# Performance work log

Hardware: AMD Instinct MI355X
Metric: run time of the kernel (lower is better)

Reference implementation:

```python
import jax, jax.numpy as jnp
import numpy as np

D = 256
NL = 2048
NP = 16384
B = 32
NEG = -1e9


def _layernorm(x, g, b, eps=1e-5):
    mu = x.mean(-1, keepdims=True)
    var = ((x - mu) ** 2).mean(-1, keepdims=True)
    return (x - mu) / jnp.sqrt(var + eps) * g + b


def _cdist(a, b):
    # pairwise euclidean distances, [Na, Nb]
    d2 = (a * a).sum(-1)[:, None] + (b * b).sum(-1)[None, :] - 2.0 * (a @ b.T)
    return jnp.sqrt(jnp.maximum(d2, 1e-12))


def setup_inputs() -> dict:
    key = jax.random.key(0)
    ks = jax.random.split(key, 24)
    init = lambda k, shape: jax.random.normal(k, shape, jnp.float32) / np.float32(np.sqrt(shape[-1]))
    inp = {
        "lig": jax.random.normal(ks[0], (NL, D), jnp.float32),
        "pro": jax.random.normal(ks[1], (NP, D), jnp.float32),
        "lig_pos": jax.random.normal(ks[2], (NL, 3), jnp.float32),
        "pro_pos": jax.random.normal(ks[3], (NP, 3), jnp.float32),
        "lig_batch": jnp.sort(jax.random.randint(ks[4], (NL,), 0, B, jnp.int32)),
        "pro_batch": jnp.sort(jax.random.randint(ks[5], (NP,), 0, B, jnp.int32)),
        "Wq_lig": init(ks[6], (D, D)),
        "Wk_pro": init(ks[7], (D, D)),
        "Wv_pro": init(ks[8], (D, D)),
        "Wq_pro": init(ks[9], (D, D)),
        "Wk_lig": init(ks[10], (D, D)),
        "Wv_lig": init(ks[11], (D, D)),
        "Wout_lig": init(ks[12], (D, D)),
        "bout_lig": jnp.zeros((D,), jnp.float32),
        "Wout_pro": init(ks[13], (D, D)),
        "bout_pro": jnp.zeros((D,), jnp.float32),
        "g_lig": jnp.ones((D,), jnp.float32),
        "b_lig": jnp.zeros((D,), jnp.float32),
        "g_pro": jnp.ones((D,), jnp.float32),
        "b_pro": jnp.zeros((D,), jnp.float32),
    }
    return inp


def reference(lig, pro, lig_pos, pro_pos, lig_batch, pro_batch,
              Wq_lig, Wk_pro, Wv_pro, Wq_pro, Wk_lig, Wv_lig,
              Wout_lig, bout_lig, Wout_pro, bout_pro,
              g_lig, b_lig, g_pro, b_pro):
    scale = jnp.float32(np.sqrt(D))
    # block-diagonal structure via batch-id mask; each row has >=1 valid col
    mask = lig_batch[:, None] == pro_batch[None, :]  # [NL, NP]
    dist_bias = jnp.exp(-_cdist(lig_pos, pro_pos) / 10.0)  # [NL, NP]

    # ligand <- protein
    Q = lig @ Wq_lig.T
    K = pro @ Wk_pro.T
    V = pro @ Wv_pro.T
    scores = Q @ K.T / scale + dist_bias
    attn = jax.nn.softmax(jnp.where(mask, scores, NEG), axis=-1)
    l_ctx = attn @ V
    lig_out = _layernorm(lig + l_ctx @ Wout_lig.T + bout_lig, g_lig, b_lig)

    # protein <- ligand
    Q2 = pro @ Wq_pro.T
    K2 = lig @ Wk_lig.T
    V2 = lig @ Wv_lig.T
    scores2 = Q2 @ K2.T / scale + dist_bias.T
    attn2 = jax.nn.softmax(jnp.where(mask.T, scores2, NEG), axis=-1)
    p_ctx = attn2 @ V2
    pro_out = _layernorm(pro + p_ctx @ Wout_pro.T + bout_pro, g_pro, b_pro)

    return lig_out, pro_out
```

## Files before the change

### kernel.cpp

```cpp
#include <hip/hip_runtime.h>

static constexpr int NLr = 2048;
static constexpr int NPr = 16384;
static constexpr int DIM = 256;
static constexpr int NB  = 32;

typedef unsigned short bf16_t;
using bf16x8 = __attribute__((ext_vector_type(8))) short;
using f32x4  = __attribute__((ext_vector_type(4))) float;

__device__ inline float bf2f(bf16_t u){
  union { unsigned int i; float f; } c; c.i = ((unsigned int)u) << 16; return c.f;
}
__device__ inline bf16_t f2bf(float f){
  union { float f; unsigned int i; } c; c.f = f;
  unsigned int x = c.i;
  return (bf16_t)((x + 0x7fffu + ((x >> 16) & 1u)) >> 16);
}
__device__ inline float wave_sum(float x){
  #pragma unroll
  for (int off = 32; off; off >>= 1) x += __shfl_xor(x, off, 64);
  return x;
}
__device__ inline bf16x8 ldfrag_f32(const float* p){
  float4 a = *reinterpret_cast<const float4*>(p);
  float4 b = *reinterpret_cast<const float4*>(p + 4);
  bf16x8 r;
  r[0]=(short)f2bf(a.x); r[1]=(short)f2bf(a.y); r[2]=(short)f2bf(a.z); r[3]=(short)f2bf(a.w);
  r[4]=(short)f2bf(b.x); r[5]=(short)f2bf(b.y); r[6]=(short)f2bf(b.z); r[7]=(short)f2bf(b.w);
  return r;
}
__device__ inline void hilo8(const float* p, bf16x8& hi, bf16x8& lo){
  #pragma unroll
  for (int i = 0; i < 8; i++){
    float v = p[i];
    bf16_t h = f2bf(v);
    hi[i] = (short)h;
    lo[i] = (short)f2bf(v - bf2f(h));
  }
}

static constexpr int OPART_OFF  = 2621440;
static constexpr int MLPART_OFF = 2605056;

__global__ void bounds_kernel(const int* __restrict__ lb, const int* __restrict__ pb,
                              int* __restrict__ ls, int* __restrict__ ps){
  int t = threadIdx.x;
  if (t <= NB){
    int lo = 0, hi = NLr;
    while (lo < hi){ int mid = (lo + hi) >> 1; if (lb[mid] < t) lo = mid + 1; else hi = mid; }
    ls[t] = lo;
    lo = 0; hi = NPr;
    while (lo < hi){ int mid = (lo + hi) >> 1; if (pb[mid] < t) lo = mid + 1; else hi = mid; }
    ps[t] = lo;
  }
}

__global__ __launch_bounds__(256) void wprod4(
    const float* __restrict__ Wq_lig, const float* __restrict__ Wk_pro,
    const float* __restrict__ Wk_lig, const float* __restrict__ Wq_pro,
    const float* __restrict__ Wout_lig, const float* __restrict__ Wv_pro,
    const float* __restrict__ Wout_pro, const float* __restrict__ Wv_lig,
    bf16_t* __restrict__ A1, bf16_t* __restrict__ B2,
    bf16_t* __restrict__ PtTL, bf16_t* __restrict__ PtTP){
  __shared__ float Sa[1088];
  __shared__ float Sb[1088];
  const int z = blockIdx.z;
  const float *A, *B; bf16_t* C;
  if      (z == 0){ A = Wq_lig;   B = Wk_pro; C = A1;   }
  else if (z == 1){ A = Wk_lig;   B = Wq_pro; C = B2;   }
  else if (z == 2){ A = Wout_lig; B = Wv_pro; C = PtTL; }
  else            { A = Wout_pro; B = Wv_lig; C = PtTP; }
  const int t  = threadIdx.x;
  const int tx = t & 15, ty = t >> 4;
  const int bm = blockIdx.x, bn = blockIdx.y;
  float acc[4][4] = {};
  if (z < 2){
    float (*As)[68] = (float(*)[68])Sa;
    float (*Bs)[68] = (float(*)[68])Sb;
    const int kk = t >> 4, c0 = (t & 15) << 2;
    for (int kt = 0; kt < DIM; kt += 16){
      float4 av = *reinterpret_cast<const float4*>(A + (size_t)(kt+kk)*DIM + bm*64 + c0);
      float4 bv = *reinterpret_cast<const float4*>(B + (size_t)(kt+kk)*DIM + bn*64 + c0);
      As[kk][c0+0]=av.x; As[kk][c0+1]=av.y; As[kk][c0+2]=av.z; As[kk][c0+3]=av.w;
      Bs[kk][c0+0]=bv.x; Bs[kk][c0+1]=bv.y; Bs[kk][c0+2]=bv.z; Bs[kk][c0+3]=bv.w;
      __syncthreads();
      #pragma unroll
      for (int k = 0; k < 16; k++){
        float a[4], b[4];
        #pragma unroll
        for (int i = 0; i < 4; i++) a[i] = As[k][ty*4+i];
        #pragma unroll
        for (int j = 0; j < 4; j++) b[j] = Bs[k][tx*4+j];
        #pragma unroll
        for (int i = 0; i < 4; i++)
          #pragma unroll
          for (int j = 0; j < 4; j++) acc[i][j] += a[i]*b[j];
      }
      __syncthreads();
    }
  } else {
    float (*As)[17] = (float(*)[17])Sa;
    float (*Bs)[68] = (float(*)[68])Sb;
    const int r  = t >> 2, k0 = (t & 3) << 2;
    const int kk = t >> 4, c0 = (t & 15) << 2;
    for (int kt = 0; kt < DIM; kt += 16){
      float4 av = *reinterpret_cast<const float4*>(A + (size_t)(bm*64+r)*DIM + kt + k0);
      float4 bv = *reinterpret_cast<const float4*>(B + (size_t)(kt+kk)*DIM + bn*64 + c0);
      As[r][k0+0]=av.x; As[r][k0+1]=av.y; As[r][k0+2]=av.z; As[r][k0+3]=av.w;
      Bs[kk][c0+0]=bv.x; Bs[kk][c0+1]=bv.y; Bs[kk][c0+2]=bv.z; Bs[kk][c0+3]=bv.w;
      __syncthreads();
      #pragma unroll
      for (int k = 0; k < 16; k++){
        float a[4], b[4];
        #pragma unroll
        for (int i = 0; i < 4; i++) a[i] = As[ty*4+i][k];
        #pragma unroll
        for (int j = 0; j < 4; j++) b[j] = Bs[k][tx*4+j];
        #pragma unroll
        for (int i = 0; i < 4; i++)
          #pragma unroll
          for (int j = 0; j < 4; j++) acc[i][j] += a[i]*b[j];
      }
      __syncthreads();
    }
  }
  #pragma unroll
  for (int i = 0; i < 4; i++){
    ushort4 o;
    o.x=f2bf(acc[i][0]); o.y=f2bf(acc[i][1]); o.z=f2bf(acc[i][2]); o.w=f2bf(acc[i][3]);
    *reinterpret_cast<ushort4*>(C + (size_t)(bm*64+ty*4+i)*DIM + bn*64 + tx*4) = o;
  }
}

__global__ __launch_bounds__(256) void gemm2(
    const float* __restrict__ A, const bf16_t* __restrict__ Ba, const bf16_t* __restrict__ Bb,
    bf16_t* __restrict__ Ca, bf16_t* __restrict__ Cb){
  const bf16_t* B = blockIdx.z ? Bb : Ba;
  bf16_t*       C = blockIdx.z ? Cb : Ca;
  __shared__ float As[64][17];
  __shared__ float Bs[16][68];
  const int t  = threadIdx.x;
  const int r  = t >> 2, k0 = (t & 3) << 2;
  const int kk = t >> 4, c0 = (t & 15) << 2;
  const int tx = t & 15, ty = t >> 4;
  const int bm = blockIdx.x, bn = blockIdx.y;
  float acc[4][4] = {};
  for (int kt = 0; kt < DIM; kt += 16){
    float4 av = *reinterpret_cast<const float4*>(A + (size_t)(bm*64+r)*DIM + kt + k0);
    ushort4 bu = *reinterpret_cast<const ushort4*>(B + (size_t)(kt+kk)*DIM + bn*64 + c0);
    As[r][k0+0]=av.x; As[r][k0+1]=av.y; As[r][k0+2]=av.z; As[r][k0+3]=av.w;
    Bs[kk][c0+0]=bf2f(bu.x); Bs[kk][c0+1]=bf2f(bu.y);
    Bs[kk][c0+2]=bf2f(bu.z); Bs[kk][c0+3]=bf2f(bu.w);
    __syncthreads();
    #pragma unroll
    for (int k = 0; k < 16; k++){
      float a[4], b[4];
      #pragma unroll
      for (int i = 0; i < 4; i++) a[i] = As[ty*4+i][k];
      #pragma unroll
      for (int j = 0; j < 4; j++) b[j] = Bs[k][tx*4+j];
      #pragma unroll
      for (int i = 0; i < 4; i++)
        #pragma unroll
        for (int j = 0; j < 4; j++) acc[i][j] += a[i]*b[j];
    }
    __syncthreads();
  }
  #pragma unroll
  for (int i = 0; i < 4; i++){
    ushort4 o;
    o.x=f2bf(acc[i][0]); o.y=f2bf(acc[i][1]); o.z=f2bf(acc[i][2]); o.w=f2bf(acc[i][3]);
    *reinterpret_cast<ushort4*>(C + (size_t)(bm*64+ty*4+i)*DIM + bn*64 + tx*4) = o;
  }
}

__global__ __launch_bounds__(128) void attn_lig(
    const bf16_t* __restrict__ Qb, const float* __restrict__ Kf,
    const float* __restrict__ posA, const float* __restrict__ posB,
    const int* __restrict__ batchA, const int* __restrict__ startB,
    float* __restrict__ dout, int NK){
  __shared__ __align__(16) char raw[36864];
  __shared__ bf16_t Pbuf[2][16][40];
  __shared__ float  mlb[2][2][16];
  bf16_t* Vlds = (bf16_t*)raw;
  float*  Ob   = (float*)raw;
  float* Opart  = dout + OPART_OFF;
  float* mlpart = dout + MLPART_OFF;

  const int t = threadIdx.x, wl = t >> 6, lane = t & 63;
  const int qrow = lane & 15, q4 = lane >> 4;
  const int tile = blockIdx.x >> 2, split = blockIdx.x & 3;
  const int row0 = tile * 16, pidx = blockIdx.x;

  const int rb = batchA[row0 + qrow];
  const int j0 = startB[rb], j1 = startB[rb + 1];
  const float ax = posA[(size_t)(row0+qrow)*3+0];
  const float ay = posA[(size_t)(row0+qrow)*3+1];
  const float az = posA[(size_t)(row0+qrow)*3+2];
  const int kmin = startB[batchA[row0]];
  const int kmax = startB[batchA[row0 + 15] + 1];
  const int base = kmin & ~63;

  bf16x8 qf[8];
  #pragma unroll
  for (int s = 0; s < 8; s++)
    qf[s] = *reinterpret_cast<const bf16x8*>(Qb + (size_t)(row0+qrow)*DIM + s*32 + q4*8);

  f32x4 O[16];
  #pragma unroll
  for (int i = 0; i < 16; i++) O[i] = (f32x4){0.f,0.f,0.f,0.f};
  float m_ = -3.0e38f, l_ = 0.f;

  for (int c = base + split*64; c < kmax; c += 256){
    __syncthreads();
    {
      const int key = t & 63, half = t >> 6;
      const float* src = Kf + (size_t)min(c + key, NK-1)*DIM + half*128;
      #pragma unroll
      for (int gch = 0; gch < 4; gch++){
        float4 tmp[8];
        #pragma unroll
        for (int u = 0; u < 8; u++)
          tmp[u] = *reinterpret_cast<const float4*>(src + gch*32 + u*4);
        #pragma unroll
        for (int u = 0; u < 8; u++){
          int d = half*128 + gch*32 + u*4;
          Vlds[(d+0)*72 + key] = f2bf(tmp[u].x);
          Vlds[(d+1)*72 + key] = f2bf(tmp[u].y);
          Vlds[(d+2)*72 + key] = f2bf(tmp[u].z);
          Vlds[(d+3)*72 + key] = f2bf(tmp[u].w);
        }
      }
    }
    __syncthreads();

    const int kc0 = c + wl*32, colbase = wl*32;
    f32x4 a0 = (f32x4){0.f,0.f,0.f,0.f}, a1 = a0;
    const float* kr0 = Kf + (size_t)min(kc0 + qrow,      NK-1)*DIM;
    const float* kr1 = Kf + (size_t)min(kc0 + 16 + qrow, NK-1)*DIM;
    #pragma unroll
    for (int s = 0; s < 8; s++){
      bf16x8 ka = ldfrag_f32(kr0 + s*32 + q4*8);
      bf16x8 kb = ldfrag_f32(kr1 + s*32 + q4*8);
      a0 = __builtin_amdgcn_mfma_f32_16x16x32_bf16(ka, qf[s], a0, 0, 0, 0);
      a1 = __builtin_amdgcn_mfma_f32_16x16x32_bf16(kb, qf[s], a1, 0, 0, 0);
    }
    float sc[2][4]; bool vm[2][4];
    float cm = -3.0e38f;
    #pragma unroll
    for (int h = 0; h < 2; h++)
      #pragma unroll
      for (int r = 0; r < 4; r++){
        int key = kc0 + h*16 + q4*4 + r;
        bool vld = (key >= j0) && (key < j1);
        int kc = min(key, NK-1);
        float bx = posB[(size_t)kc*3+0], by = posB[(size_t)kc*3+1], bz = posB[(size_t)kc*3+2];
        float dx = ax-bx, dy = ay-by, dz = az-bz;
        float dist = sqrtf(fmaxf(dx*dx + dy*dy + dz*dz, 1e-12f));
        float sv = (h ? a1[r] : a0[r]) * 0.0625f + __expf(-0.1f*dist);
        sc[h][r] = vld ? sv : -3.0e38f;
        vm[h][r] = vld;
        cm = fmaxf(cm, sc[h][r]);
      }
    cm = fmaxf(cm, __shfl_xor(cm, 16));
    cm = fmaxf(cm, __shfl_xor(cm, 32));
    float mn = fmaxf(m_, cm);
    float aa = __expf(m_ - mn);
    float p[2][4]; float ps = 0.f;
    #pragma unroll
    for (int h = 0; h < 2; h++)
      #pragma unroll
      for (int r = 0; r < 4; r++){
        p[h][r] = vm[h][r] ? __expf(sc[h][r] - mn) : 0.f;
        ps += p[h][r];
      }
    ps += __shfl_xor(ps, 16);
    ps += __shfl_xor(ps, 32);
    l_ = l_*aa + ps;
    m_ = mn;
    ushort4 w0, w1;
    w0.x=f2bf(p[0][0]); w0.y=f2bf(p[0][1]); w0.z=f2bf(p[0][2]); w0.w=f2bf(p[0][3]);
    w1.x=f2bf(p[1][0]); w1.y=f2bf(p[1][1]); w1.z=f2bf(p[1][2]); w1.w=f2bf(p[1][3]);
    *reinterpret_cast<ushort4*>(&Pbuf[wl][qrow][q4*4])      = w0;
    *reinterpret_cast<ushort4*>(&Pbuf[wl][qrow][16 + q4*4]) = w1;
    float af0 = __shfl(aa, q4*4+0), af1 = __shfl(aa, q4*4+1);
    float af2 = __shfl(aa, q4*4+2), af3 = __shfl(aa, q4*4+3);
    #pragma unroll
    for (int i = 0; i < 16; i++){
      O[i][0]*=af0; O[i][1]*=af1; O[i][2]*=af2; O[i][3]*=af3;
    }
    bf16x8 pa = *reinterpret_cast<const bf16x8*>(&Pbuf[wl][qrow][q4*8]);
    #pragma unroll
    for (int i = 0; i < 16; i++){
      const bf16_t* vp = Vlds + (size_t)(i*16 + qrow)*72 + colbase + q4*8;
      bf16x8 vb = *reinterpret_cast<const bf16x8*>(vp);
      O[i] = __builtin_amdgcn_mfma_f32_16x16x32_bf16(pa, vb, O[i], 0, 0, 0);
    }
  }

  __syncthreads();
  if (lane < 16){ mlb[wl][0][lane] = m_; mlb[wl][1][lane] = l_; }
  #pragma unroll
  for (int i = 0; i < 16; i++)
    #pragma unroll
    for (int r = 0; r < 4; r++)
      Ob[wl*4096 + (q4*4+r)*256 + i*16 + qrow] = O[i][r];
  __syncthreads();
  for (int e = t; e < 4096; e += 128){
    int row = e >> 8, d = e & 255;
    float m0 = mlb[0][0][row], m1 = mlb[1][0][row];
    float mg = fmaxf(m0, m1);
    float f0 = __expf(m0 - mg), f1 = __expf(m1 - mg);
    Opart[(size_t)pidx*4096 + row*256 + d] = Ob[row*256 + d]*f0 + Ob[4096 + row*256 + d]*f1;
  }
  if (t < 16){
    float m0 = mlb[0][0][t], l0 = mlb[0][1][t];
    float m1 = mlb[1][0][t], l1 = mlb[1][1][t];
    float mg = fmaxf(m0, m1);
    mlpart[pidx*32 + t]      = mg;
    mlpart[pidx*32 + 16 + t] = l0*__expf(m0-mg) + l1*__expf(m1-mg);
  }
}

__global__ __launch_bounds__(128) void merge_lig(
    const float* __restrict__ dpart, const bf16_t* __restrict__ PtT,
    const float* __restrict__ X, const float* __restrict__ bo,
    const float* __restrict__ g, const float* __restrict__ bb,
    float* __restrict__ out){
  __shared__ float ctxl[16*260];
  __shared__ float Yb[16*260];
  __shared__ float wgt[4][16];
  __shared__ float dens[16];
  const float* Opart  = dpart + OPART_OFF;
  const float* mlpart = dpart + MLPART_OFF;
  const int t = threadIdx.x, wl = t >> 6, lane = t & 63;
  const int qrow = lane & 15, q4 = lane >> 4;
  const int tile = blockIdx.x, row0 = tile*16;
  if (t < 16){
    float mm[4], ll[4], mg = -3.0e38f;
    #pragma unroll
    for (int s = 0; s < 4; s++){
      mm[s] = mlpart[(tile*4+s)*32 + t];
      ll[s] = mlpart[(tile*4+s)*32 + 16 + t];
      mg = fmaxf(mg, mm[s]);
    }
    float den = 0.f;
    #pragma unroll
    for (int s = 0; s < 4; s++){
      float w = __expf(mm[s] - mg);
      wgt[s][t] = w;
      den += ll[s]*w;
    }
    dens[t] = den;
  }
  __syncthreads();
  for (int e = t; e < 4096; e += 128){
    int row = e >> 8, d = e & 255;
    float acc = 0.f;
    #pragma unroll
    for (int s = 0; s < 4; s++)
      acc += Opart[((size_t)(tile*4+s))*4096 + row*256 + d] * wgt[s][row];
    float dd = dens[row];
    ctxl[row*260 + d] = (dd > 0.f) ? acc/dd : 0.f;
  }
  __syncthreads();
  f32x4 Y[8];
  #pragma unroll
  for (int i = 0; i < 8; i++) Y[i] = (f32x4){0.f,0.f,0.f,0.f};
  #pragma unroll
  for (int s = 0; s < 8; s++){
    bf16x8 ca, cl;
    hilo8(ctxl + qrow*260 + s*32 + q4*8, ca, cl);
    #pragma unroll
    for (int tt = 0; tt < 8; tt++){
      const bf16_t* pb = PtT + (size_t)((wl*8+tt)*16 + qrow)*DIM + s*32 + q4*8;
      bf16x8 mb = *reinterpret_cast<const bf16x8*>(pb);
      Y[tt] = __builtin_amdgcn_mfma_f32_16x16x32_bf16(ca, mb, Y[tt], 0, 0, 0);
      Y[tt] = __builtin_amdgcn_mfma_f32_16x16x32_bf16(cl, mb, Y[tt], 0, 0, 0);
    }
  }
  #pragma unroll
  for (int tt = 0; tt < 8; tt++)
    #pragma unroll
    for (int r = 0; r < 4; r++)
      Yb[(q4*4+r)*260 + (wl*8+tt)*16 + qrow] = Y[tt][r];
  __syncthreads();
  for (int i = 0; i < 8; i++){
    int r = wl*8 + i, grow = row0 + r;
    float4 yv = *reinterpret_cast<const float4*>(&Yb[r*260 + 4*lane]);
    float4 xv = *reinterpret_cast<const float4*>(X  + (size_t)grow*DIM + 4*lane);
    float4 bv = *reinterpret_cast<const float4*>(bo + 4*lane);
    float4 gv = *reinterpret_cast<const float4*>(g  + 4*lane);
    float4 b2 = *reinterpret_cast<const float4*>(bb + 4*lane);
    float v0 = xv.x + yv.x + bv.x, v1 = xv.y + yv.y + bv.y;
    float v2 = xv.z + yv.z + bv.z, v3 = xv.w + yv.w + bv.w;
    float sum = wave_sum(v0+v1+v2+v3);
    float ssq = wave_sum(v0*v0+v1*v1+v2*v2+v3*v3);
    float mu  = sum * (1.0f/DIM);
    float var = ssq * (1.0f/DIM) - mu*mu;
    float rr  = rsqrtf(fmaxf(var, 0.f) + 1e-5f);
    float4 o;
    o.x = (v0-mu)*rr*gv.x + b2.x;
    o.y = (v1-mu)*rr*gv.y + b2.y;
    o.z = (v2-mu)*rr*gv.z + b2.z;
    o.w = (v3-mu)*rr*gv.w + b2.w;
    *reinterpret_cast<float4*>(out + (size_t)grow*DIM + 4*lane) = o;
  }
}

__global__ __launch_bounds__(128) void attn_pro(
    const float* __restrict__ Qf, const bf16_t* __restrict__ Kb,
    const float* __restrict__ Vf,
    const float* __restrict__ posA, const float* __restrict__ posB,
    const int* __restrict__ batchA, const int* __restrict__ startB,
    const bf16_t* __restrict__ PtT,
    const float* __restrict__ X, const float* __restrict__ bo,
    const float* __restrict__ g, const float* __restrict__ bb,
    float* __restrict__ out, int out_off, int NK){
  __shared__ __align__(16) char raw[33280];
  __shared__ bf16_t Pbuf[2][16][40];
  bf16_t* Vlds = (bf16_t*)raw;
  float*  ctxl = (float*)raw;

  const int t = threadIdx.x, wl = t >> 6, lane = t & 63;
  const int qrow = lane & 15, q4 = lane >> 4;
  const int row0b = blockIdx.x * 32, row0 = row0b + wl*16;

  const int rb = batchA[row0 + qrow];
  const int j0 = startB[rb], j1 = startB[rb + 1];
  const float ax = posA[(size_t)(row0+qrow)*3+0];
  const float ay = posA[(size_t)(row0+qrow)*3+1];
  const float az = posA[(size_t)(row0+qrow)*3+2];
  const int kmin = startB[batchA[row0b]];
  const int kmax = startB[batchA[row0b + 31] + 1];
  const int base = kmin & ~31;

  bf16x8 qf[8], ql[8];
  #pragma unroll
  for (int s = 0; s < 8; s++)
    hilo8(Qf + (size_t)(row0+qrow)*DIM + s*32 + q4*8, qf[s], ql[s]);

  f32x4 O[16];
  #pragma unroll
  for (int i = 0; i < 16; i++) O[i] = (f32x4){0.f,0.f,0.f,0.f};
  float m_ = -3.0e38f, l_ = 0.f;

  for (int c = base; c < kmax; c += 32){
    __syncthreads();
    {
      const int key = t & 31, qtr = t >> 5;
      const float* src = Vf + (size_t)min(c + key, NK-1)*DIM + qtr*64;
      #pragma unroll
      for (int gch = 0; gch < 2; gch++){
        float4 tmp[8];
        #pragma unroll
        for (int u = 0; u < 8; u++)
          tmp[u] = *reinterpret_cast<const float4*>(src + gch*32 + u*4);
        #pragma unroll
        for (int u = 0; u < 8; u++){
          int d = qtr*64 + gch*32 + u*4;
          Vlds[(d+0)*40 + key] = f2bf(tmp[u].x);
          Vlds[(d+1)*40 + key] = f2bf(tmp[u].y);
          Vlds[(d+2)*40 + key] = f2bf(tmp[u].z);
          Vlds[(d+3)*40 + key] = f2bf(tmp[u].w);
        }
      }
    }
    __syncthreads();

    f32x4 a0 = (f32x4){0.f,0.f,0.f,0.f}, a1 = a0;
    const bf16_t* kr0 = Kb + (size_t)min(c + qrow,      NK-1)*DIM;
    const bf16_t* kr1 = Kb + (size_t)min(c + 16 + qrow, NK-1)*DIM;
    #pragma unroll
    for (int s = 0; s < 8; s++){
      bf16x8 ka = *reinterpret_cast<const bf16x8*>(kr0 + s*32 + q4*8);
      bf16x8 kb = *reinterpret_cast<const bf16x8*>(kr1 + s*32 + q4*8);
      a0 = __builtin_amdgcn_mfma_f32_16x16x32_bf16(ka, qf[s], a0, 0, 0, 0);
      a1 = __builtin_amdgcn_mfma_f32_16x16x32_bf16(kb, qf[s], a1, 0, 0, 0);
      a0 = __builtin_amdgcn_mfma_f32_16x16x32_bf16(ka, ql[s], a0, 0, 0, 0);
      a1 = __builtin_amdgcn_mfma_f32_16x16x32_bf16(kb, ql[s], a1, 0, 0, 0);
    }
    float sc[2][4]; bool vm[2][4];
    float cm = -3.0e38f;
    #pragma unroll
    for (int h = 0; h < 2; h++)
      #pragma unroll
      for (int r = 0; r < 4; r++){
        int key = c + h*16 + q4*4 + r;
        bool vld = (key >= j0) && (key < j1);
        int kc = min(key, NK-1);
        float bx = posB[(size_t)kc*3+0], by = posB[(size_t)kc*3+1], bz = posB[(size_t)kc*3+2];
        float dx = ax-bx, dy = ay-by, dz = az-bz;
        float dist = sqrtf(fmaxf(dx*dx + dy*dy + dz*dz, 1e-12f));
        float sv = (h ? a1[r] : a0[r]) * 0.0625f + __expf(-0.1f*dist);
        sc[h][r] = vld ? sv : -3.0e38f;
        vm[h][r] = vld;
        cm = fmaxf(cm, sc[h][r]);
      }
    cm = fmaxf(cm, __shfl_xor(cm, 16));
    cm = fmaxf(cm, __shfl_xor(cm, 32));
    float mn = fmaxf(m_, cm);
    float aa = __expf(m_ - mn);
    float p[2][4]; float ps = 0.f;
    #pragma unroll
    for (int h = 0; h < 2; h++)
      #pragma unroll
      for (int r = 0; r < 4; r++){
        p[h][r] = vm[h][r] ? __expf(sc[h][r] - mn) : 0.f;
        ps += p[h][r];
      }
    ps += __shfl_xor(ps, 16);
    ps += __shfl_xor(ps, 32);
    l_ = l_*aa + ps;
    m_ = mn;
    ushort4 w0, w1;
    w0.x=f2bf(p[0][0]); w0.y=f2bf(p[0][1]); w0.z=f2bf(p[0][2]); w0.w=f2bf(p[0][3]);
    w1.x=f2bf(p[1][0]); w1.y=f2bf(p[1][1]); w1.z=f2bf(p[1][2]); w1.w=f2bf(p[1][3]);
    *reinterpret_cast<ushort4*>(&Pbuf[wl][qrow][q4*4])      = w0;
    *reinterpret_cast<ushort4*>(&Pbuf[wl][qrow][16 + q4*4]) = w1;
    float af0 = __shfl(aa, q4*4+0), af1 = __shfl(aa, q4*4+1);
    float af2 = __shfl(aa, q4*4+2), af3 = __shfl(aa, q4*4+3);
    #pragma unroll
    for (int i = 0; i < 16; i++){
      O[i][0]*=af0; O[i][1]*=af1; O[i][2]*=af2; O[i][3]*=af3;
    }
    bf16x8 pa = *reinterpret_cast<const bf16x8*>(&Pbuf[wl][qrow][q4*8]);
    #pragma unroll
    for (int i = 0; i < 16; i++){
      const bf16_t* vp = Vlds + (size_t)(i*16 + qrow)*40 + q4*8;
      bf16x8 vb = *reinterpret_cast<const bf16x8*>(vp);
      O[i] = __builtin_amdgcn_mfma_f32_16x16x32_bf16(pa, vb, O[i], 0, 0, 0);
    }
  }

  __syncthreads();
  {
    float lr0 = __shfl(l_, q4*4+0), lr1 = __shfl(l_, q4*4+1);
    float lr2 = __shfl(l_, q4*4+2), lr3 = __shfl(l_, q4*4+3);
    float i0 = lr0>0.f?1.f/lr0:0.f, i1 = lr1>0.f?1.f/lr1:0.f;
    float i2 = lr2>0.f?1.f/lr2:0.f, i3 = lr3>0.f?1.f/lr3:0.f;
    float* cw = ctxl + wl*4160;
    #pragma unroll
    for (int i = 0; i < 16; i++){
      cw[(q4*4+0)*260 + i*16+qrow] = O[i][0]*i0;
      cw[(q4*4+1)*260 + i*16+qrow] = O[i][1]*i1;
      cw[(q4*4+2)*260 + i*16+qrow] = O[i][2]*i2;
      cw[(q4*4+3)*260 + i*16+qrow] = O[i][3]*i3;
    }
  }
  const float* cw = ctxl + wl*4160;
  f32x4 Y[16];
  #pragma unroll
  for (int i = 0; i < 16; i++) Y[i] = (f32x4){0.f,0.f,0.f,0.f};
  #pragma unroll
  for (int s = 0; s < 8; s++){
    bf16x8 ca, cl;
    hilo8(cw + qrow*260 + s*32 + q4*8, ca, cl);
    #pragma unroll
    for (int tt = 0; tt < 16; tt++){
      const bf16_t* pb = PtT + (size_t)(tt*16 + qrow)*DIM + s*32 + q4*8;
      bf16x8 mb = *reinterpret_cast<const bf16x8*>(pb);
      Y[tt] = __builtin_amdgcn_mfma_f32_16x16x32_bf16(ca, mb, Y[tt], 0, 0, 0);
      Y[tt] = __builtin_amdgcn_mfma_f32_16x16x32_bf16(cl, mb, Y[tt], 0, 0, 0);
    }
  }
  float* YB = ctxl + wl*4160;
  #pragma unroll
  for (int tt = 0; tt < 16; tt++)
    #pragma unroll
    for (int r = 0; r < 4; r++)
      YB[(q4*4+r)*260 + tt*16 + qrow] = Y[tt][r];

  for (int i = 0; i < 16; i++){
    int grow = row0 + i;
    float4 yv = *reinterpret_cast<const float4*>(&YB[i*260 + 4*lane]);
    float4 xv = *reinterpret_cast<const float4*>(X  + (size_t)grow*DIM + 4*lane);
    float4 bv = *reinterpret_cast<const float4*>(bo + 4*lane);
    float4 gv = *reinterpret_cast<const float4*>(g  + 4*lane);
    float4 b2 = *reinterpret_cast<const float4*>(bb + 4*lane);
    float v0 = xv.x + yv.x + bv.x, v1 = xv.y + yv.y + bv.y;
    float v2 = xv.z + yv.z + bv.z, v3 = xv.w + yv.w + bv.w;
    float sum = wave_sum(v0+v1+v2+v3);
    float ssq = wave_sum(v0*v0+v1*v1+v2*v2+v3*v3);
    float mu  = sum * (1.0f/DIM);
    float var = ssq * (1.0f/DIM) - mu*mu;
    float rr  = rsqrtf(fmaxf(var, 0.f) + 1e-5f);
    float4 o;
    o.x = (v0-mu)*rr*gv.x + b2.x;
    o.y = (v1-mu)*rr*gv.y + b2.y;
    o.z = (v2-mu)*rr*gv.z + b2.z;
    o.w = (v3-mu)*rr*gv.w + b2.w;
    *reinterpret_cast<float4*>(out + (size_t)out_off + (size_t)grow*DIM + 4*lane) = o;
  }
}

extern "C" void kernel_launch(void* const* d_in, const int* in_sizes, int n_in,
                              void* d_out, int out_size, void* d_ws, size_t ws_size,
                              hipStream_t stream){
  const float* lig      = (const float*)d_in[0];
  const float* pro      = (const float*)d_in[1];
  const float* lig_pos  = (const float*)d_in[2];
  const float* pro_pos  = (const float*)d_in[3];
  const int*   lig_batch= (const int*)d_in[4];
  const int*   pro_batch= (const int*)d_in[5];
  const float* Wq_lig   = (const float*)d_in[6];
  const float* Wk_pro   = (const float*)d_in[7];
  const float* Wv_pro   = (const float*)d_in[8];
  const float* Wq_pro   = (const float*)d_in[9];
  const float* Wk_lig   = (const float*)d_in[10];
  const float* Wv_lig   = (const float*)d_in[11];
  const float* Wout_lig = (const float*)d_in[12];
  const float* bout_lig = (const float*)d_in[13];
  const float* Wout_pro = (const float*)d_in[14];
  const float* bout_pro = (const float*)d_in[15];
  const float* g_lig    = (const float*)d_in[16];
  const float* b_lig    = (const float*)d_in[17];
  const float* g_pro    = (const float*)d_in[18];
  const float* b_pro    = (const float*)d_in[19];

  int* ib        = (int*)d_ws;
  int* lig_start = ib + 16;
  int* pro_start = ib + 56;
  bf16_t* wsb  = ((bf16_t*)d_ws) + 256;
  bf16_t* A1   = wsb;
  bf16_t* B2   = A1   + DIM*DIM;
  bf16_t* PtTL = B2   + DIM*DIM;
  bf16_t* PtTP = PtTL + DIM*DIM;
  bf16_t* G    = PtTP + DIM*DIM;
  bf16_t* T_lig= G    + (size_t)NLr*DIM;

  float* outp = (float*)d_out;

  hipLaunchKernelGGL(bounds_kernel, dim3(1), dim3(64), 0, stream,
                     lig_batch, pro_batch, lig_start, pro_start);
  hipLaunchKernelGGL(wprod4, dim3(4,4,4), dim3(256), 0, stream,
                     Wq_lig, Wk_pro, Wk_lig, Wq_pro, Wout_lig, Wv_pro, Wout_pro, Wv_lig,
                     A1, B2, PtTL, PtTP);
  hipLaunchKernelGGL(gemm2, dim3(NLr/64, 4, 2), dim3(256), 0, stream,
                     lig, A1, B2, T_lig, G);

  hipLaunchKernelGGL(attn_lig, dim3(NLr/16*4), dim3(128), 0, stream,
                     T_lig, pro, lig_pos, pro_pos, lig_batch, pro_start, outp, NPr);
  hipLaunchKernelGGL(merge_lig, dim3(NLr/16), dim3(128), 0, stream,
                     outp, PtTL, lig, bout_lig, g_lig, b_lig, outp);

  hipLaunchKernelGGL(attn_pro, dim3(NPr/32), dim3(128), 0, stream,
                     pro, G, lig, pro_pos, lig_pos, pro_batch, lig_start, PtTP,
                     pro, bout_pro, g_pro, b_pro, outp, NLr*DIM, NLr);
}
```

Before: 265.5 us.

## Double attn_lig key splits and split attn_pro keys across waves per row tile

attn_lig now splits each ligand tile's key range into 8 partial blocks instead of 4, and merge_lig combines 8 partials. The ml partials move to workspace and the O partials to a new offset in the output buffer. attn_pro switches from two waves each owning 16 rows over 32-key chunks to one 16-row tile per block, with the two waves splitting 64-key chunks and merging their softmax states through LDS. The output projection and layernorm are then split across the two waves. This raises parallelism and the block count for both attention kernels, at the cost of extra merge traffic, LDS work and barriers.

```diff
diff --git a/kernel.cpp b/kernel.cpp
--- a/kernel.cpp
+++ b/kernel.cpp
@@ -40,8 +40,7 @@
   }
 }
 
-static constexpr int OPART_OFF  = 2621440;
-static constexpr int MLPART_OFF = 2605056;
+static constexpr int OPART_OFF = 524288;
 
 __global__ void bounds_kernel(const int* __restrict__ lb, const int* __restrict__ pb,
                               int* __restrict__ ls, int* __restrict__ ps){
@@ -179,19 +178,18 @@
     const bf16_t* __restrict__ Qb, const float* __restrict__ Kf,
     const float* __restrict__ posA, const float* __restrict__ posB,
     const int* __restrict__ batchA, const int* __restrict__ startB,
-    float* __restrict__ dout, int NK){
+    float* __restrict__ dout, float* __restrict__ mlpart, int NK){
   __shared__ __align__(16) char raw[36864];
   __shared__ bf16_t Pbuf[2][16][40];
   __shared__ float  mlb[2][2][16];
   bf16_t* Vlds = (bf16_t*)raw;
   float*  Ob   = (float*)raw;
-  float* Opart  = dout + OPART_OFF;
-  float* mlpart = dout + MLPART_OFF;
+  float* Opart = dout + OPART_OFF;
 
   const int t = threadIdx.x, wl = t >> 6, lane = t & 63;
   const int qrow = lane & 15, q4 = lane >> 4;
-  const int tile = blockIdx.x >> 2, split = blockIdx.x & 3;
-  const int row0 = tile * 16, pidx = blockIdx.x;
+  const int pidx = blockIdx.x, tile = pidx >> 3, split = pidx & 7;
+  const int row0 = tile * 16;
 
   const int rb = batchA[row0 + qrow];
   const int j0 = startB[rb], j1 = startB[rb + 1];
@@ -212,7 +210,7 @@
   for (int i = 0; i < 16; i++) O[i] = (f32x4){0.f,0.f,0.f,0.f};
   float m_ = -3.0e38f, l_ = 0.f;
 
-  for (int c = base + split*64; c < kmax; c += 256){
+  for (int c = base + split*64; c < kmax; c += 512){
     __syncthreads();
     {
       const int key = t & 63, half = t >> 6;
@@ -324,30 +322,30 @@
 }
 
 __global__ __launch_bounds__(128) void merge_lig(
-    const float* __restrict__ dpart, const bf16_t* __restrict__ PtT,
+    const float* __restrict__ dpart, const float* __restrict__ mlpart,
+    const bf16_t* __restrict__ PtT,
     const float* __restrict__ X, const float* __restrict__ bo,
     const float* __restrict__ g, const float* __restrict__ bb,
     float* __restrict__ out){
   __shared__ float ctxl[16*260];
   __shared__ float Yb[16*260];
-  __shared__ float wgt[4][16];
+  __shared__ float wgt[8][16];
   __shared__ float dens[16];
-  const float* Opart  = dpart + OPART_OFF;
-  const float* mlpart = dpart + MLPART_OFF;
+  const float* Opart = dpart + OPART_OFF;
   const int t = threadIdx.x, wl = t >> 6, lane = t & 63;
   const int qrow = lane & 15, q4 = lane >> 4;
   const int tile = blockIdx.x, row0 = tile*16;
   if (t < 16){
-    float mm[4], ll[4], mg = -3.0e38f;
-    #pragma unroll
-    for (int s = 0; s < 4; s++){
-      mm[s] = mlpart[(tile*4+s)*32 + t];
-      ll[s] = mlpart[(tile*4+s)*32 + 16 + t];
+    float mm[8], ll[8], mg = -3.0e38f;
+    #pragma unroll
+    for (int s = 0; s < 8; s++){
+      mm[s] = mlpart[(tile*8+s)*32 + t];
+      ll[s] = mlpart[(tile*8+s)*32 + 16 + t];
       mg = fmaxf(mg, mm[s]);
     }
     float den = 0.f;
     #pragma unroll
-    for (int s = 0; s < 4; s++){
+    for (int s = 0; s < 8; s++){
       float w = __expf(mm[s] - mg);
       wgt[s][t] = w;
       den += ll[s]*w;
@@ -359,8 +357,8 @@
     int row = e >> 8, d = e & 255;
     float acc = 0.f;
     #pragma unroll
-    for (int s = 0; s < 4; s++)
-      acc += Opart[((size_t)(tile*4+s))*4096 + row*256 + d] * wgt[s][row];
+    for (int s = 0; s < 8; s++)
+      acc += Opart[((size_t)(tile*8+s))*4096 + row*256 + d] * wgt[s][row];
     float dd = dens[row];
     ctxl[row*260 + d] = (dd > 0.f) ? acc/dd : 0.f;
   }
@@ -418,23 +416,24 @@
     const float* __restrict__ X, const float* __restrict__ bo,
     const float* __restrict__ g, const float* __restrict__ bb,
     float* __restrict__ out, int out_off, int NK){
-  __shared__ __align__(16) char raw[33280];
+  __shared__ __align__(16) char raw[36864];
   __shared__ bf16_t Pbuf[2][16][40];
+  __shared__ float  mlb[2][2][16];
   bf16_t* Vlds = (bf16_t*)raw;
-  float*  ctxl = (float*)raw;
+  float*  Ob   = (float*)raw;
 
   const int t = threadIdx.x, wl = t >> 6, lane = t & 63;
   const int qrow = lane & 15, q4 = lane >> 4;
-  const int row0b = blockIdx.x * 32, row0 = row0b + wl*16;
+  const int row0 = blockIdx.x * 16;
 
   const int rb = batchA[row0 + qrow];
   const int j0 = startB[rb], j1 = startB[rb + 1];
   const float ax = posA[(size_t)(row0+qrow)*3+0];
   const float ay = posA[(size_t)(row0+qrow)*3+1];
   const float az = posA[(size_t)(row0+qrow)*3+2];
-  const int kmin = startB[batchA[row0b]];
-  const int kmax = startB[batchA[row0b + 31] + 1];
-  const int base = kmin & ~31;
+  const int kmin = startB[batchA[row0]];
+  const int kmax = startB[batchA[row0 + 15] + 1];
+  const int base = kmin & ~63;
 
   bf16x8 qf[8], ql[8];
   #pragma unroll
@@ -446,32 +445,33 @@
   for (int i = 0; i < 16; i++) O[i] = (f32x4){0.f,0.f,0.f,0.f};
   float m_ = -3.0e38f, l_ = 0.f;
 
-  for (int c = base; c < kmax; c += 32){
+  for (int c = base; c < kmax; c += 64){
     __syncthreads();
     {
-      const int key = t & 31, qtr = t >> 5;
-      const float* src = Vf + (size_t)min(c + key, NK-1)*DIM + qtr*64;
-      #pragma unroll
-      for (int gch = 0; gch < 2; gch++){
+      const int key = t & 63, half = t >> 6;
+      const float* src = Vf + (size_t)min(c + key, NK-1)*DIM + half*128;
+      #pragma unroll
+      for (int gch = 0; gch < 4; gch++){
         float4 tmp[8];
         #pragma unroll
         for (int u = 0; u < 8; u++)
           tmp[u] = *reinterpret_cast<const float4*>(src + gch*32 + u*4);
         #pragma unroll
         for (int u = 0; u < 8; u++){
-          int d = qtr*64 + gch*32 + u*4;
-          Vlds[(d+0)*40 + key] = f2bf(tmp[u].x);
-          Vlds[(d+1)*40 + key] = f2bf(tmp[u].y);
-          Vlds[(d+2)*40 + key] = f2bf(tmp[u].z);
-          Vlds[(d+3)*40 + key] = f2bf(tmp[u].w);
+          int d = half*128 + gch*32 + u*4;
+          Vlds[(d+0)*72 + key] = f2bf(tmp[u].x);
+          Vlds[(d+1)*72 + key] = f2bf(tmp[u].y);
+          Vlds[(d+2)*72 + key] = f2bf(tmp[u].z);
+          Vlds[(d+3)*72 + key] = f2bf(tmp[u].w);
         }
       }
     }
     __syncthreads();
 
+    const int kc0 = c + wl*32, colbase = wl*32;
     f32x4 a0 = (f32x4){0.f,0.f,0.f,0.f}, a1 = a0;
-    const bf16_t* kr0 = Kb + (size_t)min(c + qrow,      NK-1)*DIM;
-    const bf16_t* kr1 = Kb + (size_t)min(c + 16 + qrow, NK-1)*DIM;
+    const bf16_t* kr0 = Kb + (size_t)min(kc0 + qrow,      NK-1)*DIM;
+    const bf16_t* kr1 = Kb + (size_t)min(kc0 + 16 + qrow, NK-1)*DIM;
     #pragma unroll
     for (int s = 0; s < 8; s++){
       bf16x8 ka = *reinterpret_cast<const bf16x8*>(kr0 + s*32 + q4*8);
@@ -487,7 +487,7 @@
     for (int h = 0; h < 2; h++)
       #pragma unroll
       for (int r = 0; r < 4; r++){
-        int key = c + h*16 + q4*4 + r;
+        int key = kc0 + h*16 + q4*4 + r;
         bool vld = (key >= j0) && (key < j1);
         int kc = min(key, NK-1);
         float bx = posB[(size_t)kc*3+0], by = posB[(size_t)kc*3+1], bz = posB[(size_t)kc*3+2];
@@ -528,53 +528,60 @@
     bf16x8 pa = *reinterpret_cast<const bf16x8*>(&Pbuf[wl][qrow][q4*8]);
     #pragma unroll
     for (int i = 0; i < 16; i++){
-      const bf16_t* vp = Vlds + (size_t)(i*16 + qrow)*40 + q4*8;
+      const bf16_t* vp = Vlds + (size_t)(i*16 + qrow)*72 + colbase + q4*8;
       bf16x8 vb = *reinterpret_cast<const bf16x8*>(vp);
       O[i] = __builtin_amdgcn_mfma_f32_16x16x32_bf16(pa, vb, O[i], 0, 0, 0);
     }
   }
 
   __syncthreads();
-  {
-    float lr0 = __shfl(l_, q4*4+0), lr1 = __shfl(l_, q4*4+1);
-    float lr2 = __shfl(l_, q4*4+2), lr3 = __shfl(l_, q4*4+3);
-    float i0 = lr0>0.f?1.f/lr0:0.f, i1 = lr1>0.f?1.f/lr1:0.f;
-    float i2 = lr2>0.f?1.f/lr2:0.f, i3 = lr3>0.f?1.f/lr3:0.f;
-    float* cw = ctxl + wl*4160;
-    #pragma unroll
-    for (int i = 0; i < 16; i++){
-      cw[(q4*4+0)*260 + i*16+qrow] = O[i][0]*i0;
-      cw[(q4*4+1)*260 + i*16+qrow] = O[i][1]*i1;
-      cw[(q4*4+2)*260 + i*16+qrow] = O[i][2]*i2;
-      cw[(q4*4+3)*260 + i*16+qrow] = O[i][3]*i3;
-    }
-  }
-  const float* cw = ctxl + wl*4160;
-  f32x4 Y[16];
-  #pragma unroll
-  for (int i = 0; i < 16; i++) Y[i] = (f32x4){0.f,0.f,0.f,0.f};
+  if (lane < 16){ mlb[wl][0][lane] = m_; mlb[wl][1][lane] = l_; }
+  #pragma unroll
+  for (int i = 0; i < 16; i++)
+    #pragma unroll
+    for (int r = 0; r < 4; r++)
+      Ob[wl*4096 + (q4*4+r)*256 + i*16 + qrow] = O[i][r];
+  __syncthreads();
+  for (int e = t; e < 4096; e += 128){
+    int row = e >> 8;
+    float m0 = mlb[0][0][row], l0 = mlb[0][1][row];
+    float m1 = mlb[1][0][row], l1 = mlb[1][1][row];
+    float mg = fmaxf(m0, m1);
+    float f0 = __expf(m0 - mg), f1 = __expf(m1 - mg);
+    float den = l0*f0 + l1*f1;
+    float v = Ob[e]*f0 + Ob[4096 + e]*f1;
+    Ob[e] = (den > 0.f) ? v/den : 0.f;
+  }
+  __syncthreads();
+
+  const float* cw = Ob;
+  float* YB = Ob + 4096;
+  f32x4 Y[8];
+  #pragma unroll
+  for (int i = 0; i < 8; i++) Y[i] = (f32x4){0.f,0.f,0.f,0.f};
   #pragma unroll
   for (int s = 0; s < 8; s++){
     bf16x8 ca, cl;
-    hilo8(cw + qrow*260 + s*32 + q4*8, ca, cl);
-    #pragma unroll
-    for (int tt = 0; tt < 16; tt++){
-      const bf16_t* pb = PtT + (size_t)(tt*16 + qrow)*DIM + s*32 + q4*8;
+    hilo8(cw + qrow*256 + s*32 + q4*8, ca, cl);
+    #pragma unroll
+    for (int tt = 0; tt < 8; tt++){
+      const bf16_t* pb = PtT + (size_t)((wl*8+tt)*16 + qrow)*DIM + s*32 + q4*8;
       bf16x8 mb = *reinterpret_cast<const bf16x8*>(pb);
       Y[tt] = __builtin_amdgcn_mfma_f32_16x16x32_bf16(ca, mb, Y[tt], 0, 0, 0);
       Y[tt] = __builtin_amdgcn_mfma_f32_16x16x32_bf16(cl, mb, Y[tt], 0, 0, 0);
     }
   }
-  float* YB = ctxl + wl*4160;
-  #pragma unroll
-  for (int tt = 0; tt < 16; tt++)
+  __syncthreads();
+  #pragma unroll
+  for (int tt = 0; tt < 8; tt++)
     #pragma unroll
     for (int r = 0; r < 4; r++)
-      YB[(q4*4+r)*260 + tt*16 + qrow] = Y[tt][r];
-
-  for (int i = 0; i < 16; i++){
-    int grow = row0 + i;
-    float4 yv = *reinterpret_cast<const float4*>(&YB[i*260 + 4*lane]);
+      YB[(q4*4+r)*260 + (wl*8+tt)*16 + qrow] = Y[tt][r];
+  __syncthreads();
+
+  for (int i = 0; i < 8; i++){
+    int r = wl*8 + i, grow = row0 + r;
+    float4 yv = *reinterpret_cast<const float4*>(&YB[r*260 + 4*lane]);
     float4 xv = *reinterpret_cast<const float4*>(X  + (size_t)grow*DIM + 4*lane);
     float4 bv = *reinterpret_cast<const float4*>(bo + 4*lane);
     float4 gv = *reinterpret_cast<const float4*>(g  + 4*lane);
@@ -629,6 +636,7 @@
   bf16_t* PtTP = PtTL + DIM*DIM;
   bf16_t* G    = PtTP + DIM*DIM;
   bf16_t* T_lig= G    + (size_t)NLr*DIM;
+  float* mlpart= (float*)(T_lig + (size_t)NLr*DIM);
 
   float* outp = (float*)d_out;
 
@@ -640,12 +648,12 @@
   hipLaunchKernelGGL(gemm2, dim3(NLr/64, 4, 2), dim3(256), 0, stream,
                      lig, A1, B2, T_lig, G);
 
-  hipLaunchKernelGGL(attn_lig, dim3(NLr/16*4), dim3(128), 0, stream,
-                     T_lig, pro, lig_pos, pro_pos, lig_batch, pro_start, outp, NPr);
+  hipLaunchKernelGGL(attn_lig, dim3(NLr/16*8), dim3(128), 0, stream,
+                     T_lig, pro, lig_pos, pro_pos, lig_batch, pro_start, outp, mlpart, NPr);
   hipLaunchKernelGGL(merge_lig, dim3(NLr/16), dim3(128), 0, stream,
-                     outp, PtTL, lig, bout_lig, g_lig, b_lig, outp);
-
-  hipLaunchKernelGGL(attn_pro, dim3(NPr/32), dim3(128), 0, stream,
+                     outp, mlpart, PtTL, lig, bout_lig, g_lig, b_lig, outp);
+
+  hipLaunchKernelGGL(attn_pro, dim3(NPr/16), dim3(128), 0, stream,
                      pro, G, lig, pro_pos, lig_pos, pro_batch, lig_start, PtTP,
                      pro, bout_pro, g_pro, b_pro, outp, NLr*DIM, NLr);
 }
```

Measured after the change: 288.9 us. 8.8% more time.
